# Optimization experiments

Hardware: AMD Instinct MI355X
Metric: run time of the kernel (lower is better)

The kernel has to match this reference:

```python
import jax, jax.numpy as jnp
import numpy as np
from jax import lax


def _conv(x, w, b):
    # x: [N,C,H,W], w: [O,I,kh,kw], valid conv, stride 1
    y = lax.conv_general_dilated(x, w, (1, 1), 'VALID',
                                 dimension_numbers=('NCHW', 'OIHW', 'NCHW'))
    return y + b[None, :, None, None]


def _maxpool2(x):
    return lax.reduce_window(x, -jnp.inf, lax.max, (1, 1, 2, 2), (1, 1, 2, 2), 'VALID')


def _affine_grid(theta, H, W):
    # torch F.affine_grid, align_corners=False: pixel-center normalized coords
    dt = theta.dtype
    xs = (2.0 * jnp.arange(W, dtype=dt) + 1.0) / W - 1.0  # [W]
    ys = (2.0 * jnp.arange(H, dtype=dt) + 1.0) / H - 1.0  # [H]
    gx = (theta[:, 0, 0][:, None, None] * xs[None, None, :]
          + theta[:, 0, 1][:, None, None] * ys[None, :, None]
          + theta[:, 0, 2][:, None, None])  # [N,H,W]
    gy = (theta[:, 1, 0][:, None, None] * xs[None, None, :]
          + theta[:, 1, 1][:, None, None] * ys[None, :, None]
          + theta[:, 1, 2][:, None, None])  # [N,H,W]
    return gx, gy


def _grid_sample(img, gx, gy):
    # torch F.grid_sample, bilinear, zeros padding, align_corners=False
    N, C, H, W = img.shape
    ix = ((gx + 1.0) * W - 1.0) * 0.5
    iy = ((gy + 1.0) * H - 1.0) * 0.5
    x0 = jnp.floor(ix)
    y0 = jnp.floor(iy)
    x1 = x0 + 1.0
    y1 = y0 + 1.0
    wx1 = ix - x0
    wx0 = 1.0 - wx1
    wy1 = iy - y0
    wy0 = 1.0 - wy1
    flat = img.reshape(N, C, H * W)

    def tap(xf, yf):
        xi = xf.astype(jnp.int32)
        yi = yf.astype(jnp.int32)
        inb = (xi >= 0) & (xi < W) & (yi >= 0) & (yi < H)
        idx = jnp.clip(yi, 0, H - 1) * W + jnp.clip(xi, 0, W - 1)  # [N,H,W]
        v = jnp.take_along_axis(flat, idx.reshape(N, 1, H * W), axis=2)
        return v.reshape(N, C, H, W) * inb.astype(img.dtype)[:, None]

    out = (tap(x0, y0) * (wx0 * wy0)[:, None]
           + tap(x1, y0) * (wx1 * wy0)[:, None]
           + tap(x0, y1) * (wx0 * wy1)[:, None]
           + tap(x1, y1) * (wx1 * wy1)[:, None])
    return out


def setup_inputs() -> dict:
    key = jax.random.key(0)
    ks = jax.random.split(key, 8)
    b, n, d, c = 64, 256, 28, 3
    x = jax.random.normal(ks[0], (b, n, d, d, c), dtype=jnp.float32)
    conv1_w = jax.random.normal(ks[1], (8, 3, 7, 7), dtype=jnp.float32) * 0.08
    conv1_b = jnp.zeros((8,), dtype=jnp.float32)
    conv2_w = jax.random.normal(ks[2], (10, 8, 5, 5), dtype=jnp.float32) * 0.07
    conv2_b = jnp.zeros((10,), dtype=jnp.float32)
    fc1_w = jax.random.normal(ks[3], (32, 90), dtype=jnp.float32) * 0.1
    fc1_b = jnp.zeros((32,), dtype=jnp.float32)
    # fc2 initialized near identity transform (as in the torch module),
    # with a small perturbation so theta depends on the input
    fc2_w = jax.random.normal(ks[4], (6, 32), dtype=jnp.float32) * 0.01
    fc2_b = jnp.array([1.0, 0.0, 0.0, 0.0, 1.0, 0.0], dtype=jnp.float32)
    return {"x": x, "conv1_w": conv1_w, "conv1_b": conv1_b,
            "conv2_w": conv2_w, "conv2_b": conv2_b,
            "fc1_w": fc1_w, "fc1_b": fc1_b,
            "fc2_w": fc2_w, "fc2_b": fc2_b}


def reference(x, conv1_w, conv1_b, conv2_w, conv2_b, fc1_w, fc1_b, fc2_w, fc2_b):
    b, n, d, _, c = x.shape
    xi = x.reshape(-1, d, d, c).transpose(0, 3, 1, 2)  # [b*n, 3, 28, 28]
    # localization net: conv -> maxpool -> relu, twice
    h = jax.nn.relu(_maxpool2(_conv(xi, conv1_w, conv1_b)))   # [N,8,11,11]
    h = jax.nn.relu(_maxpool2(_conv(h, conv2_w, conv2_b)))    # [N,10,3,3]
    h = h.reshape(-1, 10 * 3 * 3)
    h = jax.nn.relu(h @ fc1_w.T + fc1_b)
    theta = (h @ fc2_w.T + fc2_b).reshape(-1, 2, 3)
    gx, gy = _affine_grid(theta, d, d)
    out = _grid_sample(xi, gx, gy)                            # [N,3,28,28]
    return out.transpose(0, 2, 3, 1).reshape(b, n, d, d, c)
```

## Files before the change

kernel.cpp:

```cpp
#include <hip/hip_runtime.h>


typedef _Float16 half2_t __attribute__((ext_vector_type(2)));

static __device__ inline half2_t h2(uint32_t u) {
    union { uint32_t u; half2_t h; } cv; cv.u = u; return cv.h;
}
static __device__ inline uint32_t packh2(float a, float b) {
    union { half2_t h; uint32_t u; } cv;
    cv.h = (half2_t){(_Float16)a, (_Float16)b};
    return cv.u;
}

#if __has_builtin(__builtin_amdgcn_fdot2)
#define FDOT2(a, b, c) __builtin_amdgcn_fdot2((a), (b), (c), false)
#else
#define FDOT2(a, b, c) ((float)(a)[0] * (float)(b)[0] + (float)(a)[1] * (float)(b)[1] + (c))
#endif

__launch_bounds__(256, 4)
__global__ void stn_loc_kernel(
    const float* __restrict__ x,
    const float* __restrict__ w1, const float* __restrict__ b1,
    const float* __restrict__ w2, const float* __restrict__ b2,
    const float* __restrict__ fc1w, const float* __restrict__ fc1b,
    const float* __restrict__ fc2w, const float* __restrict__ fc2b,
    float* __restrict__ theta_ws)
{
    __shared__ __align__(16) _Float16 s_imgh[4][3 * 28 * 40];
    __shared__ __align__(16) uint32_t s_w1p[8 * 21 * 4];
    __shared__ __align__(16) float s_h1[4][8 * 11 * 12];
    __shared__ float s_h2[4][90];
    __shared__ float s_fch[4][32];

    const int t = threadIdx.x;
    const int nb = blockIdx.x;

    for (int im = 0; im < 4; ++im) {
        const float* img = x + ((size_t)(nb * 4 + im)) * 2352;
        for (int p = t; p < 784; p += 256) {
            const int h = p / 28, w = p - 28 * h;
            s_imgh[im][(0 * 28 + h) * 40 + w] = (_Float16)img[3 * p + 0];
            s_imgh[im][(1 * 28 + h) * 40 + w] = (_Float16)img[3 * p + 1];
            s_imgh[im][(2 * 28 + h) * 40 + w] = (_Float16)img[3 * p + 2];
        }
        for (int idx = t; idx < 504; idx += 256) {
            const int cc = idx / 168;
            const int rem = idx - 168 * cc;
            const int hh = rem / 6;
            const int kk = rem - 6 * hh;
            ((uint32_t*)s_imgh[im])[(((cc * 28 + hh) * 40) + 28 + 2 * kk) >> 1] = 0u;
        }
    }
    for (int idx = t; idx < 672; idx += 256) {
        const int o = idx / 84;  const int rem = idx - 84 * o;
        const int c = rem / 28;  const int r2 = rem - 28 * c;
        const int kh = r2 >> 2;  const int p = r2 & 3;
        const int k0 = 2 * p;
        const float* wbase = &w1[((o * 3 + c) * 7 + kh) * 7];
        const float wa = wbase[k0];
        const float wb = (k0 + 1 < 7) ? wbase[k0 + 1] : 0.0f;
        s_w1p[idx] = packh2(wa, wb);
    }
    __syncthreads();

    for (int u = t; u < 704; u += 256) {
        const int im = u / 176;
        const int r  = u - 176 * im;
        const int i = r >> 3, o = r & 7;
        float acc[22];
        #pragma unroll
        for (int j = 0; j < 22; ++j) acc[j] = 0.0f;

        for (int c = 0; c < 3; ++c) {
            #pragma unroll
            for (int kh = 0; kh < 7; ++kh) {
                const uint32_t* rowu =
                    (const uint32_t*)&s_imgh[im][(c * 28 + i + kh) * 40];
                uint32_t E[16];
                {
                    const uint4 a = ((const uint4*)rowu)[0];
                    const uint4 b = ((const uint4*)rowu)[1];
                    const uint4 cq = ((const uint4*)rowu)[2];
                    const uint4 d = ((const uint4*)rowu)[3];
                    E[0] = a.x;  E[1] = a.y;  E[2] = a.z;  E[3] = a.w;
                    E[4] = b.x;  E[5] = b.y;  E[6] = b.z;  E[7] = b.w;
                    E[8] = cq.x; E[9] = cq.y; E[10] = cq.z; E[11] = cq.w;
                    E[12] = d.x; E[13] = d.y; E[14] = d.z; E[15] = d.w;
                }
                uint32_t O[14];
                #pragma unroll
                for (int k = 0; k < 14; ++k)
                    O[k] = (E[k] >> 16) | (E[k + 1] << 16);

                const uint4 wq = *(const uint4*)&s_w1p[(o * 21 + c * 7 + kh) * 4];
                const half2_t wp0 = h2(wq.x), wp1 = h2(wq.y);
                const half2_t wp2 = h2(wq.z), wp3 = h2(wq.w);

                #pragma unroll
                for (int j = 0; j < 22; j += 2) {
                    const int b0 = j >> 1;
                    acc[j]     = FDOT2(h2(E[b0]),     wp0, acc[j]);
                    acc[j]     = FDOT2(h2(E[b0 + 1]), wp1, acc[j]);
                    acc[j]     = FDOT2(h2(E[b0 + 2]), wp2, acc[j]);
                    acc[j]     = FDOT2(h2(E[b0 + 3]), wp3, acc[j]);
                    acc[j + 1] = FDOT2(h2(O[b0]),     wp0, acc[j + 1]);
                    acc[j + 1] = FDOT2(h2(O[b0 + 1]), wp1, acc[j + 1]);
                    acc[j + 1] = FDOT2(h2(O[b0 + 2]), wp2, acc[j + 1]);
                    acc[j + 1] = FDOT2(h2(O[b0 + 3]), wp3, acc[j + 1]);
                }
            }
        }
        const float bias = b1[o];
        float hm[11];
        #pragma unroll
        for (int j = 0; j < 11; ++j) hm[j] = fmaxf(acc[2 * j], acc[2 * j + 1]);
        #pragma unroll
        for (int j = 0; j < 11; ++j) {
            float v = __shfl_xor(hm[j], 8);
            hm[j] = fmaxf(hm[j], v);
        }
        if ((i & 1) == 0) {
            float* row = &s_h1[im][(o * 11 + (i >> 1)) * 12];
            #pragma unroll
            for (int j = 0; j < 11; ++j) row[j] = fmaxf(hm[j] + bias, 0.0f);
        }
    }
    __syncthreads();

    if (t < 240) {
        const int im = t / 60;
        const int r = t - 60 * im;
        const int o = r / 6, i = r - 6 * (r / 6);
        float acc2[6];
        const float bias = b2[o];
        #pragma unroll
        for (int j = 0; j < 6; ++j) acc2[j] = bias;
        for (int c = 0; c < 8; ++c) {
            #pragma unroll
            for (int kh = 0; kh < 5; ++kh) {
                const float* hrow = &s_h1[im][(c * 11 + i + kh) * 12];
                float im2[12];
                #pragma unroll
                for (int qq = 0; qq < 3; ++qq) {
                    float4 v = ((const float4*)hrow)[qq];
                    im2[4 * qq + 0] = v.x; im2[4 * qq + 1] = v.y;
                    im2[4 * qq + 2] = v.z; im2[4 * qq + 3] = v.w;
                }
                const float* wr = &w2[(o * 8 + c) * 25 + kh * 5];
                float wv[5];
                #pragma unroll
                for (int qq = 0; qq < 5; ++qq) wv[qq] = wr[qq];
                #pragma unroll
                for (int kw = 0; kw < 5; ++kw) {
                    #pragma unroll
                    for (int j = 0; j < 6; ++j)
                        acc2[j] += im2[j + kw] * wv[kw];
                }
            }
        }
        float hp[3];
        #pragma unroll
        for (int qq = 0; qq < 3; ++qq) hp[qq] = fmaxf(acc2[2 * qq], acc2[2 * qq + 1]);
        #pragma unroll
        for (int qq = 0; qq < 3; ++qq) {
            float v = __shfl_xor(hp[qq], 1);
            hp[qq] = fmaxf(hp[qq], v);
        }
        if ((i & 1) == 0) {
            #pragma unroll
            for (int qq = 0; qq < 3; ++qq)
                s_h2[im][o * 9 + (i >> 1) * 3 + qq] = fmaxf(hp[qq], 0.0f);
        }
    }
    __syncthreads();

    {
        const int im = t >> 6;
        const int of = (t >> 1) & 31;
        const int l = t & 1;
        float acc = 0.0f;
        const float* wr = &fc1w[of * 90];
        #pragma unroll
        for (int j = 0; j < 45; ++j) {
            const int jj = l + 2 * j;
            acc += s_h2[im][jj] * wr[jj];
        }
        acc += __shfl_xor(acc, 1);
        if (l == 0) s_fch[im][of] = fmaxf(acc + fc1b[of], 0.0f);
    }
    __syncthreads();

    if (t < 192) {
        const int im = t / 48;
        const int r = t - 48 * im;
        const int of = r >> 3, l = r & 7;
        float acc = 0.0f;
        const float* wr = &fc2w[of * 32];
        #pragma unroll
        for (int m = 0; m < 4; ++m) {
            const int j = l + 8 * m;
            acc += s_fch[im][j] * wr[j];
        }
        acc += __shfl_xor(acc, 1);
        acc += __shfl_xor(acc, 2);
        acc += __shfl_xor(acc, 4);
        if (l == 0) theta_ws[((size_t)(nb * 4 + im)) * 6 + of] = acc + fc2b[of];
    }
}

__launch_bounds__(256)
__global__ void stn_sample_kernel(
    const float* __restrict__ x,
    const float* __restrict__ theta_ws,
    float* __restrict__ out)
{
    const int t = threadIdx.x;
    const int n = blockIdx.x;
    const float* tw = theta_ws + (size_t)n * 6;
    const float t00 = tw[0], t01 = tw[1], t02 = tw[2];
    const float t10 = tw[3], t11 = tw[4], t12 = tw[5];
    const float* img = x + (size_t)n * 2352;
    float* outp = out + (size_t)n * 2352;

    for (int p = t; p < 784; p += 256) {
        int h = p / 28, w = p - 28 * h;
        float xs = (2.0f * w + 1.0f) * (1.0f / 28.0f) - 1.0f;
        float ys = (2.0f * h + 1.0f) * (1.0f / 28.0f) - 1.0f;
        float gx = t00 * xs + t01 * ys + t02;
        float gy = t10 * xs + t11 * ys + t12;
        float ix = ((gx + 1.0f) * 28.0f - 1.0f) * 0.5f;
        float iy = ((gy + 1.0f) * 28.0f - 1.0f) * 0.5f;
        float x0f = floorf(ix), y0f = floorf(iy);
        float wx1 = ix - x0f, wx0 = 1.0f - wx1;
        float wy1 = iy - y0f, wy0 = 1.0f - wy1;
        int x0 = (int)x0f, y0 = (int)y0f;
        int x1 = x0 + 1, y1 = y0 + 1;
        float fx0 = (x0 >= 0 && x0 < 28) ? 1.0f : 0.0f;
        float fx1 = (x1 >= 0 && x1 < 28) ? 1.0f : 0.0f;
        float fy0 = (y0 >= 0 && y0 < 28) ? 1.0f : 0.0f;
        float fy1 = (y1 >= 0 && y1 < 28) ? 1.0f : 0.0f;
        float w00 = wx0 * wy0 * fx0 * fy0;
        float w10 = wx1 * wy0 * fx1 * fy0;
        float w01 = wx0 * wy1 * fx0 * fy1;
        float w11 = wx1 * wy1 * fx1 * fy1;
        int cx0 = min(max(x0, 0), 27), cx1 = min(max(x1, 0), 27);
        int cy0 = min(max(y0, 0), 27), cy1 = min(max(y1, 0), 27);
        const float* p00 = img + (cy0 * 28 + cx0) * 3;
        const float* p10 = img + (cy0 * 28 + cx1) * 3;
        const float* p01 = img + (cy1 * 28 + cx0) * 3;
        const float* p11 = img + (cy1 * 28 + cx1) * 3;
        float* o3 = outp + 3 * p;
        #pragma unroll
        for (int c = 0; c < 3; ++c) {
            o3[c] = p00[c] * w00 + p10[c] * w10 + p01[c] * w01 + p11[c] * w11;
        }
    }
}

extern "C" void kernel_launch(void* const* d_in, const int* in_sizes, int n_in,
                              void* d_out, int out_size, void* d_ws, size_t ws_size,
                              hipStream_t stream) {
    const float* x     = (const float*)d_in[0];
    const float* w1    = (const float*)d_in[1];
    const float* b1    = (const float*)d_in[2];
    const float* w2    = (const float*)d_in[3];
    const float* b2    = (const float*)d_in[4];
    const float* fc1w  = (const float*)d_in[5];
    const float* fc1b  = (const float*)d_in[6];
    const float* fc2w  = (const float*)d_in[7];
    const float* fc2b  = (const float*)d_in[8];
    float* outp  = (float*)d_out;
    float* theta = (float*)d_ws;

    const int n_img = 64 * 256;
    stn_loc_kernel<<<dim3(n_img / 4), dim3(256), 0, stream>>>(
        x, w1, b1, w2, b2, fc1w, fc1b, fc2w, fc2b, theta);
    stn_sample_kernel<<<dim3(n_img), dim3(256), 0, stream>>>(x, theta, outp);
}
```

Baseline: 312.3 us.

## Compute conv1 with MFMA 16x16x32 f16 instead of fdot2 loops

Reformulates the first 7x7 convolution as a matrix multiply on MFMA units. Weights are staged in shared memory as A-fragments, with K padded to 32 per step and output channels padded to 16. Each wavefront handles one image and builds B-fragments from unaligned 64-bit shared loads combined by shifts. Pooling is done with lane shuffles on the accumulator. The padding wastes some MFMA work, but the aim is to cut the large VALU fdot2 instruction count of the old loop.

```diff
diff --git a/kernel.cpp b/kernel.cpp
--- a/kernel.cpp
+++ b/kernel.cpp
@@ -1,22 +1,8 @@
 #include <hip/hip_runtime.h>
 
 
-typedef _Float16 half2_t __attribute__((ext_vector_type(2)));
-
-static __device__ inline half2_t h2(uint32_t u) {
-    union { uint32_t u; half2_t h; } cv; cv.u = u; return cv.h;
-}
-static __device__ inline uint32_t packh2(float a, float b) {
-    union { half2_t h; uint32_t u; } cv;
-    cv.h = (half2_t){(_Float16)a, (_Float16)b};
-    return cv.u;
-}
-
-#if __has_builtin(__builtin_amdgcn_fdot2)
-#define FDOT2(a, b, c) __builtin_amdgcn_fdot2((a), (b), (c), false)
-#else
-#define FDOT2(a, b, c) ((float)(a)[0] * (float)(b)[0] + (float)(a)[1] * (float)(b)[1] + (c))
-#endif
+typedef _Float16 f16x8 __attribute__((ext_vector_type(8)));
+typedef float f32x4 __attribute__((ext_vector_type(4)));
 
 __launch_bounds__(256, 4)
 __global__ void stn_loc_kernel(
@@ -27,8 +13,8 @@
     const float* __restrict__ fc2w, const float* __restrict__ fc2b,
     float* __restrict__ theta_ws)
 {
-    __shared__ __align__(16) _Float16 s_imgh[4][3 * 28 * 40];
-    __shared__ __align__(16) uint32_t s_w1p[8 * 21 * 4];
+    __shared__ uint2 s_img64[4 * 840];
+    __shared__ __align__(16) _Float16 s_afrag[6 * 64 * 8];
     __shared__ __align__(16) float s_h1[4][8 * 11 * 12];
     __shared__ float s_h2[4][90];
     __shared__ float s_fch[4][32];
@@ -38,92 +24,110 @@
 
     for (int im = 0; im < 4; ++im) {
         const float* img = x + ((size_t)(nb * 4 + im)) * 2352;
+        _Float16* imh = ((_Float16*)s_img64) + im * 3360;
         for (int p = t; p < 784; p += 256) {
             const int h = p / 28, w = p - 28 * h;
-            s_imgh[im][(0 * 28 + h) * 40 + w] = (_Float16)img[3 * p + 0];
-            s_imgh[im][(1 * 28 + h) * 40 + w] = (_Float16)img[3 * p + 1];
-            s_imgh[im][(2 * 28 + h) * 40 + w] = (_Float16)img[3 * p + 2];
+            imh[(0 * 28 + h) * 40 + w] = (_Float16)img[3 * p + 0];
+            imh[(1 * 28 + h) * 40 + w] = (_Float16)img[3 * p + 1];
+            imh[(2 * 28 + h) * 40 + w] = (_Float16)img[3 * p + 2];
         }
         for (int idx = t; idx < 504; idx += 256) {
             const int cc = idx / 168;
             const int rem = idx - 168 * cc;
             const int hh = rem / 6;
             const int kk = rem - 6 * hh;
-            ((uint32_t*)s_imgh[im])[(((cc * 28 + hh) * 40) + 28 + 2 * kk) >> 1] = 0u;
-        }
-    }
-    for (int idx = t; idx < 672; idx += 256) {
-        const int o = idx / 84;  const int rem = idx - 84 * o;
-        const int c = rem / 28;  const int r2 = rem - 28 * c;
-        const int kh = r2 >> 2;  const int p = r2 & 3;
-        const int k0 = 2 * p;
-        const float* wbase = &w1[((o * 3 + c) * 7 + kh) * 7];
-        const float wa = wbase[k0];
-        const float wb = (k0 + 1 < 7) ? wbase[k0 + 1] : 0.0f;
-        s_w1p[idx] = packh2(wa, wb);
-    }
-    __syncthreads();
-
-    for (int u = t; u < 704; u += 256) {
-        const int im = u / 176;
-        const int r  = u - 176 * im;
-        const int i = r >> 3, o = r & 7;
-        float acc[22];
-        #pragma unroll
-        for (int j = 0; j < 22; ++j) acc[j] = 0.0f;
-
-        for (int c = 0; c < 3; ++c) {
+            ((uint32_t*)imh)[(((cc * 28 + hh) * 40) + 28 + 2 * kk) >> 1] = 0u;
+        }
+    }
+    for (int d = t; d < 3072; d += 256) {
+        const int ks = d >> 9;
+        const int ln = (d >> 3) & 63;
+        const int j  = d & 7;
+        const int o  = ln & 15;
+        const int pp = ln >> 4;
+        const int pair = ks * 4 + pp;
+        float v = 0.0f;
+        if (o < 8 && pair < 21 && j < 7) {
+            const int c = pair / 7, kh = pair - 7 * c;
+            v = w1[((o * 3 + c) * 7 + kh) * 7 + j];
+        }
+        s_afrag[(ks * 64 + ln) * 8 + j] = (_Float16)v;
+    }
+    __syncthreads();
+
+    {
+        const int l  = t & 63;
+        const int wv = t >> 6;
+        const int p  = l >> 4;
+        const int nn = l & 15;
+        const int yoff = nn >> 3;
+        const int xx = nn & 7;
+
+        f16x8 af[6];
+        #pragma unroll
+        for (int ks = 0; ks < 6; ++ks)
+            af[ks] = *(const f16x8*)&s_afrag[(ks * 64 + l) * 8];
+
+        int poff[6];
+        #pragma unroll
+        for (int ks = 0; ks < 6; ++ks) {
+            const int pair = ks * 4 + p;
+            if (pair < 21) {
+                const int c = pair / 7, kh = pair - 7 * c;
+                poff[ks] = (c * 28 + kh) * 80;
+            } else {
+                poff[ks] = 0;
+            }
+        }
+        const int base0 = wv * 6720 + yoff * 80 + xx * 2;
+
+        float bia[4];
+        #pragma unroll
+        for (int r = 0; r < 4; ++r) bia[r] = b1[(p & 1) * 4 + r];
+
+        for (int yt = 0; yt < 11; ++yt) {
             #pragma unroll
-            for (int kh = 0; kh < 7; ++kh) {
-                const uint32_t* rowu =
-                    (const uint32_t*)&s_imgh[im][(c * 28 + i + kh) * 40];
-                uint32_t E[16];
-                {
-                    const uint4 a = ((const uint4*)rowu)[0];
-                    const uint4 b = ((const uint4*)rowu)[1];
-                    const uint4 cq = ((const uint4*)rowu)[2];
-                    const uint4 d = ((const uint4*)rowu)[3];
-                    E[0] = a.x;  E[1] = a.y;  E[2] = a.z;  E[3] = a.w;
-                    E[4] = b.x;  E[5] = b.y;  E[6] = b.z;  E[7] = b.w;
-                    E[8] = cq.x; E[9] = cq.y; E[10] = cq.z; E[11] = cq.w;
-                    E[12] = d.x; E[13] = d.y; E[14] = d.z; E[15] = d.w;
-                }
-                uint32_t O[14];
-                #pragma unroll
-                for (int k = 0; k < 14; ++k)
-                    O[k] = (E[k] >> 16) | (E[k + 1] << 16);
-
-                const uint4 wq = *(const uint4*)&s_w1p[(o * 21 + c * 7 + kh) * 4];
-                const half2_t wp0 = h2(wq.x), wp1 = h2(wq.y);
-                const half2_t wp2 = h2(wq.z), wp3 = h2(wq.w);
-
-                #pragma unroll
-                for (int j = 0; j < 22; j += 2) {
-                    const int b0 = j >> 1;
-                    acc[j]     = FDOT2(h2(E[b0]),     wp0, acc[j]);
-                    acc[j]     = FDOT2(h2(E[b0 + 1]), wp1, acc[j]);
-                    acc[j]     = FDOT2(h2(E[b0 + 2]), wp2, acc[j]);
-                    acc[j]     = FDOT2(h2(E[b0 + 3]), wp3, acc[j]);
-                    acc[j + 1] = FDOT2(h2(O[b0]),     wp0, acc[j + 1]);
-                    acc[j + 1] = FDOT2(h2(O[b0 + 1]), wp1, acc[j + 1]);
-                    acc[j + 1] = FDOT2(h2(O[b0 + 2]), wp2, acc[j + 1]);
-                    acc[j + 1] = FDOT2(h2(O[b0 + 3]), wp3, acc[j + 1]);
+            for (int xt = 0; xt < 3; ++xt) {
+                f32x4 acc = {0.0f, 0.0f, 0.0f, 0.0f};
+                #pragma unroll
+                for (int ks = 0; ks < 6; ++ks) {
+                    const int s = base0 + poff[ks] + yt * 160 + xt * 16;
+                    const int idx = s >> 3;
+                    const uint2 d0 = s_img64[idx];
+                    const uint2 d1 = s_img64[idx + 1];
+                    const uint2 d2 = s_img64[idx + 2];
+                    const uint32_t shb = (uint32_t)(s & 2) * 8u;
+                    const bool qq = (s & 4) != 0;
+                    const uint32_t e0 = (uint32_t)(((((uint64_t)d0.y) << 32) | d0.x) >> shb);
+                    const uint32_t e1 = (uint32_t)(((((uint64_t)d1.x) << 32) | d0.y) >> shb);
+                    const uint32_t e2 = (uint32_t)(((((uint64_t)d1.y) << 32) | d1.x) >> shb);
+                    const uint32_t e3 = (uint32_t)(((((uint64_t)d2.x) << 32) | d1.y) >> shb);
+                    const uint32_t e4 = (uint32_t)(((((uint64_t)d2.y) << 32) | d2.x) >> shb);
+                    union { uint32_t u[4]; f16x8 h; } bf;
+                    bf.u[0] = qq ? e1 : e0;
+                    bf.u[1] = qq ? e2 : e1;
+                    bf.u[2] = qq ? e3 : e2;
+                    bf.u[3] = qq ? e4 : e3;
+                    acc = __builtin_amdgcn_mfma_f32_16x16x32_f16(af[ks], bf.h, acc, 0, 0, 0);
+                }
+                float pv[4];
+                #pragma unroll
+                for (int r = 0; r < 4; ++r) {
+                    const float a_ = acc[r];
+                    const float vb = __shfl_xor(a_, 8);
+                    const float m1 = fmaxf(a_, vb);
+                    const float hc = __shfl_xor(m1, 1);
+                    pv[r] = fmaxf(m1, hc);
+                }
+                if (p < 2 && (nn & 9) == 0 && !(xt == 2 && xx >= 6)) {
+                    const int pc = xt * 4 + (xx >> 1);
+                    #pragma unroll
+                    for (int r = 0; r < 4; ++r) {
+                        const int o = p * 4 + r;
+                        s_h1[wv][(o * 11 + yt) * 12 + pc] = fmaxf(pv[r] + bia[r], 0.0f);
+                    }
                 }
             }
-        }
-        const float bias = b1[o];
-        float hm[11];
-        #pragma unroll
-        for (int j = 0; j < 11; ++j) hm[j] = fmaxf(acc[2 * j], acc[2 * j + 1]);
-        #pragma unroll
-        for (int j = 0; j < 11; ++j) {
-            float v = __shfl_xor(hm[j], 8);
-            hm[j] = fmaxf(hm[j], v);
-        }
-        if ((i & 1) == 0) {
-            float* row = &s_h1[im][(o * 11 + (i >> 1)) * 12];
-            #pragma unroll
-            for (int j = 0; j < 11; ++j) row[j] = fmaxf(hm[j] + bias, 0.0f);
         }
     }
     __syncthreads();
@@ -148,14 +152,14 @@
                     im2[4 * qq + 2] = v.z; im2[4 * qq + 3] = v.w;
                 }
                 const float* wr = &w2[(o * 8 + c) * 25 + kh * 5];
-                float wv[5];
-                #pragma unroll
-                for (int qq = 0; qq < 5; ++qq) wv[qq] = wr[qq];
+                float wv5[5];
+                #pragma unroll
+                for (int qq = 0; qq < 5; ++qq) wv5[qq] = wr[qq];
                 #pragma unroll
                 for (int kw = 0; kw < 5; ++kw) {
                     #pragma unroll
                     for (int j = 0; j < 6; ++j)
-                        acc2[j] += im2[j + kw] * wv[kw];
+                        acc2[j] += im2[j + kw] * wv5[kw];
                 }
             }
         }
```

After: 356.6 us. 1.14x slower.

## Pack conv2 activations and weights as fp16 channel pairs and use fdot2

Applied to the files above, without the earlier changes.

Stores the pooled conv1 output in shared memory as fp16 pairs interleaved across channel pairs, keeping only the 10 rows and columns that conv2 reads. Conv2 weights are pre-packed into shared memory as half2 channel pairs, and the conv2 inner loop uses fdot2, halving the multiply-accumulate count and removing global weight loads from the loop. It also swaps the shift/or used to build odd conv1 windows for an alignbit instruction, and moves the conv2 bias to after pooling. This cuts FLOPs and shared-memory traffic in conv2 at the cost of lower intermediate precision, which only affects the localization net that produces theta.

```diff
diff --git a/kernel.cpp b/kernel.cpp
--- a/kernel.cpp
+++ b/kernel.cpp
@@ -16,6 +16,12 @@
 #define FDOT2(a, b, c) __builtin_amdgcn_fdot2((a), (b), (c), false)
 #else
 #define FDOT2(a, b, c) ((float)(a)[0] * (float)(b)[0] + (float)(a)[1] * (float)(b)[1] + (c))
+#endif
+
+#if __has_builtin(__builtin_amdgcn_alignbit)
+#define ALIGN16(hi, lo) __builtin_amdgcn_alignbit((hi), (lo), 16)
+#else
+#define ALIGN16(hi, lo) (((lo) >> 16) | ((hi) << 16))
 #endif
 
 __launch_bounds__(256, 4)
@@ -29,7 +35,8 @@
 {
     __shared__ __align__(16) _Float16 s_imgh[4][3 * 28 * 40];
     __shared__ __align__(16) uint32_t s_w1p[8 * 21 * 4];
-    __shared__ __align__(16) float s_h1[4][8 * 11 * 12];
+    __shared__ __align__(16) uint32_t s_h1p[4 * 4 * 10 * 12];
+    __shared__ __align__(16) uint32_t s_w2h[10 * 100];
     __shared__ float s_h2[4][90];
     __shared__ float s_fch[4][32];
 
@@ -61,6 +68,16 @@
         const float wa = wbase[k0];
         const float wb = (k0 + 1 < 7) ? wbase[k0 + 1] : 0.0f;
         s_w1p[idx] = packh2(wa, wb);
+    }
+    for (int k = t; k < 1000; k += 256) {
+        const int o = k / 100;
+        const int rem = k - 100 * o;
+        const int c2kh = rem / 5;
+        const int kw = rem - 5 * c2kh;
+        const int c2 = c2kh / 5;
+        const int kh = c2kh - 5 * c2;
+        s_w2h[k] = packh2(w2[((o * 8 + 2 * c2) * 5 + kh) * 5 + kw],
+                          w2[((o * 8 + 2 * c2 + 1) * 5 + kh) * 5 + kw]);
     }
     __syncthreads();
 
@@ -91,7 +108,7 @@
                 uint32_t O[14];
                 #pragma unroll
                 for (int k = 0; k < 14; ++k)
-                    O[k] = (E[k] >> 16) | (E[k + 1] << 16);
+                    O[k] = ALIGN16(E[k + 1], E[k]);
 
                 const uint4 wq = *(const uint4*)&s_w1p[(o * 21 + c * 7 + kh) * 4];
                 const half2_t wp0 = h2(wq.x), wp1 = h2(wq.y);
@@ -120,10 +137,13 @@
             float v = __shfl_xor(hm[j], 8);
             hm[j] = fmaxf(hm[j], v);
         }
-        if ((i & 1) == 0) {
-            float* row = &s_h1[im][(o * 11 + (i >> 1)) * 12];
+        if ((i & 1) == 0 && i < 20) {
+            const int c2 = o >> 1, u2 = i >> 1;
+            _Float16* dst = ((_Float16*)s_h1p)
+                          + (((im * 4 + c2) * 10 + u2) * 12) * 2 + (o & 1);
             #pragma unroll
-            for (int j = 0; j < 11; ++j) row[j] = fmaxf(hm[j] + bias, 0.0f);
+            for (int m = 0; m < 10; ++m)
+                dst[2 * m] = (_Float16)fmaxf(hm[m] + bias, 0.0f);
         }
     }
     __syncthreads();
@@ -133,44 +153,50 @@
         const int r = t - 60 * im;
         const int o = r / 6, i = r - 6 * (r / 6);
         float acc2[6];
-        const float bias = b2[o];
-        #pragma unroll
-        for (int j = 0; j < 6; ++j) acc2[j] = bias;
-        for (int c = 0; c < 8; ++c) {
+        #pragma unroll
+        for (int j = 0; j < 6; ++j) acc2[j] = 0.0f;
+        #pragma unroll
+        for (int c2 = 0; c2 < 4; ++c2) {
             #pragma unroll
             for (int kh = 0; kh < 5; ++kh) {
-                const float* hrow = &s_h1[im][(c * 11 + i + kh) * 12];
-                float im2[12];
+                const uint32_t* row = &s_h1p[((im * 4 + c2) * 10 + (i + kh)) * 12];
+                uint32_t E[12];
+                {
+                    const uint4 a = ((const uint4*)row)[0];
+                    const uint4 b = ((const uint4*)row)[1];
+                    const uint4 cq = ((const uint4*)row)[2];
+                    E[0] = a.x;  E[1] = a.y;  E[2] = a.z;  E[3] = a.w;
+                    E[4] = b.x;  E[5] = b.y;  E[6] = b.z;  E[7] = b.w;
+                    E[8] = cq.x; E[9] = cq.y; E[10] = cq.z; E[11] = cq.w;
+                }
+                const uint32_t* wb = &s_w2h[o * 100 + (c2 * 5 + kh) * 5];
+                const half2_t w0 = h2(wb[0]), w1_ = h2(wb[1]), w2_ = h2(wb[2]),
+                              w3_ = h2(wb[3]), w4_ = h2(wb[4]);
                 #pragma unroll
-                for (int qq = 0; qq < 3; ++qq) {
-                    float4 v = ((const float4*)hrow)[qq];
-                    im2[4 * qq + 0] = v.x; im2[4 * qq + 1] = v.y;
-                    im2[4 * qq + 2] = v.z; im2[4 * qq + 3] = v.w;
-                }
-                const float* wr = &w2[(o * 8 + c) * 25 + kh * 5];
-                float wv[5];
-                #pragma unroll
-                for (int qq = 0; qq < 5; ++qq) wv[qq] = wr[qq];
-                #pragma unroll
-                for (int kw = 0; kw < 5; ++kw) {
-                    #pragma unroll
-                    for (int j = 0; j < 6; ++j)
-                        acc2[j] += im2[j + kw] * wv[kw];
+                for (int j = 0; j < 6; ++j) {
+                    float a_ = acc2[j];
+                    a_ = FDOT2(h2(E[j]),     w0,  a_);
+                    a_ = FDOT2(h2(E[j + 1]), w1_, a_);
+                    a_ = FDOT2(h2(E[j + 2]), w2_, a_);
+                    a_ = FDOT2(h2(E[j + 3]), w3_, a_);
+                    a_ = FDOT2(h2(E[j + 4]), w4_, a_);
+                    acc2[j] = a_;
                 }
             }
         }
+        const float bias = b2[o];
         float hp[3];
         #pragma unroll
-        for (int qq = 0; qq < 3; ++qq) hp[qq] = fmaxf(acc2[2 * qq], acc2[2 * qq + 1]);
-        #pragma unroll
-        for (int qq = 0; qq < 3; ++qq) {
-            float v = __shfl_xor(hp[qq], 1);
-            hp[qq] = fmaxf(hp[qq], v);
+        for (int q = 0; q < 3; ++q) hp[q] = fmaxf(acc2[2 * q], acc2[2 * q + 1]);
+        #pragma unroll
+        for (int q = 0; q < 3; ++q) {
+            float v = __shfl_xor(hp[q], 1);
+            hp[q] = fmaxf(hp[q], v);
         }
         if ((i & 1) == 0) {
             #pragma unroll
-            for (int qq = 0; qq < 3; ++qq)
-                s_h2[im][o * 9 + (i >> 1) * 3 + qq] = fmaxf(hp[qq], 0.0f);
+            for (int q = 0; q < 3; ++q)
+                s_h2[im][o * 9 + (i >> 1) * 3 + q] = fmaxf(hp[q] + bias, 0.0f);
         }
     }
     __syncthreads();
```

After: 285.1 us. -8.7%, faster.
